# Performance work log

Measured on AMD Instinct MI355X. Metric: run time of the kernel, lower is better.

The kernel has to match this reference:

```python
import jax, jax.numpy as jnp
import numpy as np

P = 2048
D = 1024
H = 16
DH = D // H
HID = 32


def setup_inputs() -> dict:
    key = jax.random.key(0)
    ks = jax.random.split(key, 10)
    s = 0.02
    return {
        "x": jax.random.normal(ks[0], (P, D), jnp.float32),
        "rel": jax.random.normal(ks[1], (P, P, 2), jnp.float32),
        "w_qkv": jax.random.normal(ks[2], (D, 3 * D), jnp.float32) * s,
        "w_proj": jax.random.normal(ks[3], (D, D), jnp.float32) * s,
        "rpb_w1": jax.random.normal(ks[4], (2, HID), jnp.float32) * s,
        "rpb_b1": jnp.zeros((HID,), jnp.float32),
        "rpb_w2": jax.random.normal(ks[5], (HID, HID), jnp.float32) * s,
        "rpb_b2": jnp.zeros((HID,), jnp.float32),
        "rpb_w3": jax.random.normal(ks[6], (HID, 1), jnp.float32) * s,
        "rpb_b3": jnp.zeros((1,), jnp.float32),
    }


def reference(x, rel, w_qkv, w_proj, rpb_w1, rpb_b1, rpb_w2, rpb_b2, rpb_w3, rpb_b3):
    scale = 1.0 / np.sqrt(DH)
    qkv = x @ w_qkv                                   # [P, 3D]
    q, k, v = jnp.split(qkv, 3, axis=-1)
    # [P, D] -> [H, P, DH]
    q = q.reshape(P, H, DH).transpose(1, 0, 2)
    k = k.reshape(P, H, DH).transpose(1, 0, 2)
    v = v.reshape(P, H, DH).transpose(1, 0, 2)
    logits = jnp.einsum('hpd,hqd->hpq', q, k) * scale  # [H, P, P]
    # RelPosBias MLP: (dx,dy) -> scalar, applied over [P, P, 2]
    hcur = jax.nn.relu(rel @ rpb_w1 + rpb_b1)
    hcur = jax.nn.relu(hcur @ rpb_w2 + rpb_b2)
    bias = (hcur @ rpb_w3 + rpb_b3)[..., 0]            # [P, P]
    logits = logits + bias[None]
    attn = jax.nn.softmax(logits, axis=-1)
    out = jnp.einsum('hpq,hqd->hpd', attn, v)          # [H, P, DH]
    out = out.transpose(1, 0, 2).reshape(P, D)
    return out @ w_proj
```

## Files before the change

### kernel.cpp

```cpp
#include <hip/hip_runtime.h>
#include <hip/hip_bf16.h>
#include <type_traits>

typedef __attribute__((ext_vector_type(8))) short bf16x8;
typedef __attribute__((ext_vector_type(4))) float floatx4;
typedef __attribute__((ext_vector_type(2))) float float2v;

__device__ __forceinline__ float bf2f(unsigned short u) {
    union { unsigned int x; float f; } v; v.x = ((unsigned int)u) << 16; return v.f;
}
__device__ __forceinline__ unsigned short f2bf(float f) {
    union { float f; unsigned int u; } v; v.f = f;
    unsigned int x = v.u;
    unsigned int r = x + 0x7fffu + ((x >> 16) & 1u);
    return (unsigned short)(r >> 16);
}

typedef const __attribute__((address_space(1))) unsigned int u32_g;
typedef __attribute__((address_space(3))) unsigned int u32_l;
__device__ __forceinline__ void gld_lds16(const void* g, void* l) {
    __builtin_amdgcn_global_load_lds((u32_g*)g, (u32_l*)l, 16, 0, 0);
}

__device__ __forceinline__ void trans32(const float* __restrict__ in,
                                        unsigned short* __restrict__ out,
                                        int K, int N, int bx, int by,
                                        unsigned short (*T)[33]) {
    const int n0 = bx * 32, k0 = by * 32;
    const int r = threadIdx.x >> 3;
    const int c4 = (threadIdx.x & 7) * 4;
    float4 v = *reinterpret_cast<const float4*>(in + (size_t)(k0 + r) * N + n0 + c4);
    T[c4 + 0][r] = f2bf(v.x);
    T[c4 + 1][r] = f2bf(v.y);
    T[c4 + 2][r] = f2bf(v.z);
    T[c4 + 3][r] = f2bf(v.w);
    __syncthreads();
    ushort4 o = {T[r][c4], T[r][c4 + 1], T[r][c4 + 2], T[r][c4 + 3]};
    *reinterpret_cast<ushort4*>(out + (size_t)(n0 + r) * K + k0 + c4) = o;
}

__global__ __launch_bounds__(256) void prep(const float* __restrict__ x,
                                            unsigned short* __restrict__ xb,
                                            const float* __restrict__ wq,
                                            unsigned short* __restrict__ wqT,
                                            const float* __restrict__ wp,
                                            unsigned short* __restrict__ wpT) {
    __shared__ unsigned short T[32][33];
    const int b = blockIdx.x;
    if (b < 1024) {
        size_t i = ((size_t)b * 256 + threadIdx.x) * 8;
        float4 a = *reinterpret_cast<const float4*>(x + i);
        float4 c = *reinterpret_cast<const float4*>(x + i + 4);
        unsigned short t[8] = {f2bf(a.x), f2bf(a.y), f2bf(a.z), f2bf(a.w),
                               f2bf(c.x), f2bf(c.y), f2bf(c.z), f2bf(c.w)};
        *reinterpret_cast<uint4*>(xb + i) = *reinterpret_cast<const uint4*>(t);
    } else if (b < 4096) {
        int t = b - 1024;
        trans32(wq, wqT, 1024, 3072, t % 96, t / 96, T);
    } else {
        int t = b - 4096;
        trans32(wp, wpT, 1024, 1024, t % 32, t / 32, T);
    }
}

__global__ __launch_bounds__(256) void gemm128(const unsigned short* __restrict__ A,
                                               const unsigned short* __restrict__ Bt,
                                               unsigned short* __restrict__ C,
                                               int M, int N, int K) {
    __shared__ __align__(16) unsigned short As[128 * 32];
    __shared__ __align__(16) unsigned short Bs[128 * 32];

    const int tid = threadIdx.x;
    const int wave = tid >> 6;
    const int lane = tid & 63;
    const int m15 = lane & 15;
    const int quad = lane >> 4;
    const int wm = wave >> 1;
    const int wn = wave & 1;
    const int m0 = blockIdx.y * 128;
    const int n0 = blockIdx.x * 128;

    const int srow = lane >> 2;
    const int scol = (lane & 3) * 8;

    floatx4 acc[4][4];
#pragma unroll
    for (int mt = 0; mt < 4; mt++)
#pragma unroll
        for (int nt = 0; nt < 4; nt++) acc[mt][nt] = {0.f, 0.f, 0.f, 0.f};

    for (int k0 = 0; k0 < K; k0 += 32) {
#pragma unroll
        for (int i = 0; i < 2; i++) {
            int j = wave * 2 + i;
            gld_lds16(A + (size_t)(m0 + j * 16 + srow) * K + k0 + scol, &As[j * 16 * 32]);
            gld_lds16(Bt + (size_t)(n0 + j * 16 + srow) * K + k0 + scol, &Bs[j * 16 * 32]);
        }
        __syncthreads();

        bf16x8 a[4];
#pragma unroll
        for (int mt = 0; mt < 4; mt++)
            a[mt] = *reinterpret_cast<bf16x8*>(&As[(wm * 64 + mt * 16 + m15) * 32 + quad * 8]);
#pragma unroll
        for (int nt = 0; nt < 4; nt++) {
            bf16x8 b = *reinterpret_cast<bf16x8*>(&Bs[(wn * 64 + nt * 16 + m15) * 32 + quad * 8]);
#pragma unroll
            for (int mt = 0; mt < 4; mt++)
                acc[mt][nt] = __builtin_amdgcn_mfma_f32_16x16x32_bf16(a[mt], b, acc[mt][nt], 0, 0, 0);
        }
        __syncthreads();
    }

#pragma unroll
    for (int mt = 0; mt < 4; mt++)
#pragma unroll
        for (int nt = 0; nt < 4; nt++)
#pragma unroll
            for (int i = 0; i < 4; i++) {
                int row = m0 + wm * 64 + mt * 16 + quad * 4 + i;
                int col = n0 + wn * 64 + nt * 16 + m15;
                C[(size_t)row * N + col] = f2bf(acc[mt][nt][i]);
            }
}

template<int BN, typename TC>
__global__ __launch_bounds__(256) void gemm_abt(const unsigned short* __restrict__ A,
                                                const unsigned short* __restrict__ Bt,
                                                TC* __restrict__ C,
                                                int M, int N, int K) {
    constexpr int NT = BN / 32;
    __shared__ __align__(16) unsigned short As[64 * 32];
    __shared__ __align__(16) unsigned short Bs[BN * 32];

    const int tid = threadIdx.x;
    const int wave = tid >> 6;
    const int lane = tid & 63;
    const int m15 = lane & 15;
    const int quad = lane >> 4;
    const int wm = wave >> 1;
    const int wn = wave & 1;
    const int m0 = blockIdx.y * 64;
    const int n0 = blockIdx.x * BN;

    const int srow = lane >> 2;
    const int scol = (lane & 3) * 8;

    floatx4 acc[2][NT];
#pragma unroll
    for (int mt = 0; mt < 2; mt++)
#pragma unroll
        for (int nt = 0; nt < NT; nt++) acc[mt][nt] = {0.f, 0.f, 0.f, 0.f};

    for (int k0 = 0; k0 < K; k0 += 32) {
        gld_lds16(A + (size_t)(m0 + wave * 16 + srow) * K + k0 + scol, &As[wave * 16 * 32]);
#pragma unroll
        for (int i = 0; i < BN / 64; i++) {
            int j = wave * (BN / 64) + i;
            gld_lds16(Bt + (size_t)(n0 + j * 16 + srow) * K + k0 + scol, &Bs[j * 16 * 32]);
        }
        __syncthreads();

        bf16x8 a[2];
#pragma unroll
        for (int mt = 0; mt < 2; mt++)
            a[mt] = *reinterpret_cast<bf16x8*>(&As[(wm * 32 + mt * 16 + m15) * 32 + quad * 8]);
#pragma unroll
        for (int nt = 0; nt < NT; nt++) {
            bf16x8 b = *reinterpret_cast<bf16x8*>(&Bs[(wn * (BN / 2) + nt * 16 + m15) * 32 + quad * 8]);
#pragma unroll
            for (int mt = 0; mt < 2; mt++)
                acc[mt][nt] = __builtin_amdgcn_mfma_f32_16x16x32_bf16(a[mt], b, acc[mt][nt], 0, 0, 0);
        }
        __syncthreads();
    }

#pragma unroll
    for (int mt = 0; mt < 2; mt++)
#pragma unroll
        for (int nt = 0; nt < NT; nt++)
#pragma unroll
            for (int i = 0; i < 4; i++) {
                int row = m0 + wm * 32 + mt * 16 + quad * 4 + i;
                int col = n0 + wn * (BN / 2) + nt * 16 + m15;
                if constexpr (std::is_same<TC, float>::value)
                    C[(size_t)row * N + col] = acc[mt][nt][i];
                else
                    C[(size_t)row * N + col] = f2bf(acc[mt][nt][i]);
            }
}

__global__ __launch_bounds__(256) void rpb_mfma_kernel(const float* __restrict__ rel,
                                                       const float* __restrict__ w1,
                                                       const float* __restrict__ b1,
                                                       const float* __restrict__ w2,
                                                       const float* __restrict__ b2,
                                                       const float* __restrict__ w3,
                                                       const float* __restrict__ b3,
                                                       unsigned short* __restrict__ biasb) {
    const int tid = threadIdx.x;
    const int wave = tid >> 6;
    const int lane = tid & 63;
    const int m15 = lane & 15;
    const int quad = lane >> 4;

    bf16x8 af0, af1;
    {
        unsigned short t0[8], t1[8];
#pragma unroll
        for (int j = 0; j < 8; j++) {
            int k = quad * 8 + j;
            t0[j] = f2bf(w2[k * 32 + m15]);
            t1[j] = f2bf(w2[k * 32 + 16 + m15]);
        }
        af0 = *reinterpret_cast<bf16x8*>(t0);
        af1 = *reinterpret_cast<bf16x8*>(t1);
    }

    float2v w1a2[4], w1b2[4], b12[4];
#pragma unroll
    for (int p = 0; p < 4; p++) {
        int base = quad * 8 + 2 * p;
        w1a2[p] = {w1[base], w1[base + 1]};
        w1b2[p] = {w1[32 + base], w1[32 + base + 1]};
        b12[p]  = {b1[base], b1[base + 1]};
    }

    floatx4 b2r0, b2r1;
    float2v w3p00, w3p01, w3p10, w3p11;
    const float LOG2E = 1.44269504f;
    {
        float4 t0 = *reinterpret_cast<const float4*>(b2 + quad * 4);
        float4 t1 = *reinterpret_cast<const float4*>(b2 + 16 + quad * 4);
        b2r0 = {t0.x, t0.y, t0.z, t0.w};
        b2r1 = {t1.x, t1.y, t1.z, t1.w};
        float4 u0 = *reinterpret_cast<const float4*>(w3 + quad * 4);
        float4 u1 = *reinterpret_cast<const float4*>(w3 + 16 + quad * 4);
        w3p00 = {u0.x * LOG2E, u0.y * LOG2E};
        w3p01 = {u0.z * LOG2E, u0.w * LOG2E};
        w3p10 = {u1.x * LOG2E, u1.y * LOG2E};
        w3p11 = {u1.z * LOG2E, u1.w * LOG2E};
    }
    const float b3s = b3[0] * LOG2E;
    const float2v z2 = {0.f, 0.f};

    const int base = blockIdx.x * 1024 + wave * 64;

    for (int it = 0; it < 4; ++it) {
        const int pix0 = base + it * 256;
#pragma unroll
        for (int t = 0; t < 4; t++) {
            const int px = pix0 + t * 16;
            float2 dxy = *reinterpret_cast<const float2*>(rel + (size_t)(px + m15) * 2);
            float2v dx2 = {dxy.x, dxy.x}, dy2 = {dxy.y, dxy.y};

            unsigned int hp[4];
#pragma unroll
            for (int p = 0; p < 4; p++) {
                float2v h = __builtin_elementwise_fma(dx2, w1a2[p],
                             __builtin_elementwise_fma(dy2, w1b2[p], b12[p]));
                h = __builtin_elementwise_max(h, z2);
                hp[p] = __builtin_amdgcn_perm(__float_as_uint(h.y), __float_as_uint(h.x), 0x07060302u);
            }
            bf16x8 hb = *reinterpret_cast<bf16x8*>(hp);

            floatx4 d0 = __builtin_amdgcn_mfma_f32_16x16x32_bf16(af0, hb, b2r0, 0, 0, 0);
            floatx4 d1 = __builtin_amdgcn_mfma_f32_16x16x32_bf16(af1, hb, b2r1, 0, 0, 0);

            float2v m00 = __builtin_elementwise_max(__builtin_shufflevector(d0, d0, 0, 1), z2);
            float2v m01 = __builtin_elementwise_max(__builtin_shufflevector(d0, d0, 2, 3), z2);
            float2v m10 = __builtin_elementwise_max(__builtin_shufflevector(d1, d1, 0, 1), z2);
            float2v m11 = __builtin_elementwise_max(__builtin_shufflevector(d1, d1, 2, 3), z2);
            float2v acc2 = m00 * w3p00;
            acc2 = __builtin_elementwise_fma(m01, w3p01, acc2);
            acc2 = __builtin_elementwise_fma(m10, w3p10, acc2);
            acc2 = __builtin_elementwise_fma(m11, w3p11, acc2);
            float s = acc2.x + acc2.y;

            s += __shfl_xor(s, 16);
            s += __shfl_xor(s, 32);
            s += b3s;

            if (quad == t)
                biasb[(size_t)pix0 + m15 * 4 + t] = f2bf(s);
        }
    }
}

__global__ __launch_bounds__(512, 4) void attn_kernel(const unsigned short* __restrict__ qkv,
                                                      const unsigned short* __restrict__ biasb,
                                                      unsigned short* __restrict__ attn_out) {
    const int h = blockIdx.x;
    const int q0 = blockIdx.y * 64;
    __shared__ __align__(16) unsigned short Kst[2][64 * 72];
    __shared__ __align__(16) unsigned short Vst[2][64 * 72];
    __shared__ __align__(16) unsigned short Ps[8][16 * 72];

    const int tid = threadIdx.x;
    const int g = tid >> 8;
    const int w = (tid >> 6) & 3;
    const int lane = tid & 63;
    const int ltid = tid & 255;
    const int m15 = lane & 15;
    const int quad = lane >> 4;

    bf16x8 qf[2];
#pragma unroll
    for (int kh = 0; kh < 2; kh++)
        qf[kh] = *reinterpret_cast<const bf16x8*>(
            qkv + (size_t)(q0 + w * 16 + m15) * 3072 + h * 64 + kh * 32 + quad * 8);

    const int kr0 = ltid >> 3, kd0 = (ltid & 7) * 8;
    const int ka = (ltid & 31) * 2;
    const int vd0 = (ltid >> 5) * 8;

    unsigned short* Kc = Kst[g];
    unsigned short* Vc = Vst[g];
    const size_t kofs = (size_t)g * 1024;

    uint4 kreg0 = *reinterpret_cast<const uint4*>(qkv + (kofs + kr0) * 3072 + 1024 + h * 64 + kd0);
    uint4 kreg1 = *reinterpret_cast<const uint4*>(qkv + (kofs + kr0 + 32) * 3072 + 1024 + h * 64 + kd0);
    uint4 vrega = *reinterpret_cast<const uint4*>(qkv + (kofs + ka) * 3072 + 2048 + h * 64 + vd0);
    uint4 vregb = *reinterpret_cast<const uint4*>(qkv + (kofs + ka + 1) * 3072 + 2048 + h * 64 + vd0);

    unsigned short br[16];
#pragma unroll
    for (int i = 0; i < 4; i++) {
        ushort4 t = *reinterpret_cast<const ushort4*>(
            biasb + (size_t)(q0 + w * 16 + quad * 4 + i) * 2048 + kofs + m15 * 4);
        br[0 * 4 + i] = t.x; br[1 * 4 + i] = t.y; br[2 * 4 + i] = t.z; br[3 * 4 + i] = t.w;
    }

    float rs[4] = {0.f, 0.f, 0.f, 0.f};
    floatx4 acc[4];
#pragma unroll
    for (int i = 0; i < 4; i++) acc[i] = {0.f, 0.f, 0.f, 0.f};
    const float c1 = 0.125f * 1.44269504f;

    for (int kt = 0; kt < 16; ++kt) {
        __syncthreads();

        *reinterpret_cast<uint4*>(&Kc[kr0 * 72 + kd0]) = kreg0;
        *reinterpret_cast<uint4*>(&Kc[(kr0 + 32) * 72 + kd0]) = kreg1;
        {
            const unsigned int* aw = reinterpret_cast<const unsigned int*>(&vrega);
            const unsigned int* bw = reinterpret_cast<const unsigned int*>(&vregb);
#pragma unroll
            for (int wd = 0; wd < 4; wd++) {
                unsigned int lo = __builtin_amdgcn_perm(bw[wd], aw[wd], 0x05040100u);
                unsigned int hi = __builtin_amdgcn_perm(bw[wd], aw[wd], 0x07060302u);
                *reinterpret_cast<unsigned int*>(&Vc[(vd0 + 2 * wd) * 72 + ka]) = lo;
                *reinterpret_cast<unsigned int*>(&Vc[(vd0 + 2 * wd + 1) * 72 + ka]) = hi;
            }
        }
        __syncthreads();

        if (kt < 15) {
            const size_t kb = kofs + (size_t)(kt + 1) * 64;
            kreg0 = *reinterpret_cast<const uint4*>(qkv + (kb + kr0) * 3072 + 1024 + h * 64 + kd0);
            kreg1 = *reinterpret_cast<const uint4*>(qkv + (kb + kr0 + 32) * 3072 + 1024 + h * 64 + kd0);
            vrega = *reinterpret_cast<const uint4*>(qkv + (kb + ka) * 3072 + 2048 + h * 64 + vd0);
            vregb = *reinterpret_cast<const uint4*>(qkv + (kb + ka + 1) * 3072 + 2048 + h * 64 + vd0);
        }

        floatx4 s[4];
#pragma unroll
        for (int nt = 0; nt < 4; nt++) s[nt] = {0.f, 0.f, 0.f, 0.f};
#pragma unroll
        for (int kh = 0; kh < 2; kh++) {
#pragma unroll
            for (int nt = 0; nt < 4; nt++) {
                bf16x8 b = *reinterpret_cast<bf16x8*>(&Kc[(nt * 16 + m15) * 72 + kh * 32 + quad * 8]);
                s[nt] = __builtin_amdgcn_mfma_f32_16x16x32_bf16(qf[kh], b, s[nt], 0, 0, 0);
            }
        }

        float p[4][4];
#pragma unroll
        for (int nt = 0; nt < 4; nt++)
#pragma unroll
            for (int i = 0; i < 4; i++) {
                float lg = fmaf(s[nt][i], c1, bf2f(br[nt * 4 + i]));
                p[nt][i] = __builtin_amdgcn_exp2f(lg);
                rs[i] += p[nt][i];
            }

        if (kt < 15) {
            const size_t kb = kofs + (size_t)(kt + 1) * 64;
#pragma unroll
            for (int i = 0; i < 4; i++) {
                ushort4 t = *reinterpret_cast<const ushort4*>(
                    biasb + (size_t)(q0 + w * 16 + quad * 4 + i) * 2048 + kb + m15 * 4);
                br[0 * 4 + i] = t.x; br[1 * 4 + i] = t.y; br[2 * 4 + i] = t.z; br[3 * 4 + i] = t.w;
            }
        }

        unsigned short* Pw = Ps[tid >> 6];
#pragma unroll
        for (int nt = 0; nt < 4; nt++)
#pragma unroll
            for (int i = 0; i < 4; i++)
                Pw[(quad * 4 + i) * 72 + nt * 16 + m15] = f2bf(p[nt][i]);
        __asm__ volatile("s_waitcnt lgkmcnt(0)" ::: "memory");

#pragma unroll
        for (int kh = 0; kh < 2; kh++) {
            bf16x8 a = *reinterpret_cast<bf16x8*>(&Pw[m15 * 72 + kh * 32 + quad * 8]);
#pragma unroll
            for (int nt = 0; nt < 4; nt++) {
                bf16x8 b = *reinterpret_cast<bf16x8*>(&Vc[(nt * 16 + m15) * 72 + kh * 32 + quad * 8]);
                acc[nt] = __builtin_amdgcn_mfma_f32_16x16x32_bf16(a, b, acc[nt], 0, 0, 0);
            }
        }
    }

    float rsum[4];
#pragma unroll
    for (int i = 0; i < 4; i++) {
        float r = rs[i];
        r += __shfl_xor(r, 1);
        r += __shfl_xor(r, 2);
        r += __shfl_xor(r, 4);
        r += __shfl_xor(r, 8);
        rsum[i] = r;
    }

    float* accbuf = reinterpret_cast<float*>(&Kst[0][0]);
    float* lbuf = accbuf + 4096;

    __syncthreads();
    if (g == 1) {
#pragma unroll
        for (int nt = 0; nt < 4; nt++)
#pragma unroll
            for (int i = 0; i < 4; i++)
                accbuf[(w * 16 + quad * 4 + i) * 64 + nt * 16 + m15] = acc[nt][i];
        if (m15 == 0) {
#pragma unroll
            for (int i = 0; i < 4; i++) lbuf[w * 16 + quad * 4 + i] = rsum[i];
        }
    }
    __syncthreads();
    if (g == 0) {
        float linv[4];
#pragma unroll
        for (int i = 0; i < 4; i++)
            linv[i] = 1.f / (rsum[i] + lbuf[w * 16 + quad * 4 + i]);
#pragma unroll
        for (int nt = 0; nt < 4; nt++)
#pragma unroll
            for (int i = 0; i < 4; i++) {
                float o = (acc[nt][i] + accbuf[(w * 16 + quad * 4 + i) * 64 + nt * 16 + m15]) * linv[i];
                int row = q0 + w * 16 + quad * 4 + i;
                int col = h * 64 + nt * 16 + m15;
                attn_out[(size_t)row * 1024 + col] = f2bf(o);
            }
    }
}

extern "C" void kernel_launch(void* const* d_in, const int* in_sizes, int n_in,
                              void* d_out, int out_size, void* d_ws, size_t ws_size,
                              hipStream_t stream) {
    const float* x      = (const float*)d_in[0];
    const float* rel    = (const float*)d_in[1];
    const float* w_qkv  = (const float*)d_in[2];
    const float* w_proj = (const float*)d_in[3];
    const float* w1     = (const float*)d_in[4];
    const float* b1     = (const float*)d_in[5];
    const float* w2     = (const float*)d_in[6];
    const float* b2     = (const float*)d_in[7];
    const float* w3     = (const float*)d_in[8];
    const float* b3     = (const float*)d_in[9];

    char* ws = (char*)d_ws;
    unsigned short* qkv   = (unsigned short*)ws;
    unsigned short* biasb = (unsigned short*)(ws + 12582912);
    unsigned short* xb    = (unsigned short*)(ws + 20971520);
    unsigned short* attn  = xb;
    unsigned short* wqT   = (unsigned short*)(ws + 25165824);
    unsigned short* wpT   = (unsigned short*)(ws + 31457280);
    float* out = (float*)d_out;

    prep<<<5120, 256, 0, stream>>>(x, xb, w_qkv, wqT, w_proj, wpT);
    gemm128<<<dim3(24, 16), 256, 0, stream>>>(xb, wqT, qkv, 2048, 3072, 1024);
    rpb_mfma_kernel<<<4096, 256, 0, stream>>>(rel, w1, b1, w2, b2, w3, b3, biasb);
    attn_kernel<<<dim3(16, 32), 512, 0, stream>>>(qkv, biasb, attn);
    gemm_abt<64, float><<<dim3(16, 32), 256, 0, stream>>>(attn, wpT, out, 2048, 1024, 1024);
}
```

Before: 232.0 us.

## Merge QKV GEMM and RPB MLP into one launch; prefetch rel, MFMA reduction

Merges the QKV projection GEMM and the relative-position-bias MLP into a single kernel that picks its role by block index, so the 384 GEMM blocks and the 4096 bias blocks run concurrently and one launch is saved. Inside the bias path, the rel coordinates for the next iteration are prefetched into registers. The cross-quad shuffle reduction is replaced by an MFMA against a ones vector that also adds the final bias. The MFMA reduction rounds partial sums to bf16 before summing, which adds precision loss, and the GEMM shape is now hardcoded.

```diff
diff --git a/kernel.cpp b/kernel.cpp
--- a/kernel.cpp
+++ b/kernel.cpp
@@ -63,13 +63,11 @@
     }
 }
 
-__global__ __launch_bounds__(256) void gemm128(const unsigned short* __restrict__ A,
-                                               const unsigned short* __restrict__ Bt,
-                                               unsigned short* __restrict__ C,
-                                               int M, int N, int K) {
-    __shared__ __align__(16) unsigned short As[128 * 32];
-    __shared__ __align__(16) unsigned short Bs[128 * 32];
-
+__device__ __forceinline__ void gemm128_body(const unsigned short* __restrict__ A,
+                                             const unsigned short* __restrict__ Bt,
+                                             unsigned short* __restrict__ C,
+                                             int bx, int by,
+                                             unsigned short* As, unsigned short* Bs) {
     const int tid = threadIdx.x;
     const int wave = tid >> 6;
     const int lane = tid & 63;
@@ -77,9 +75,8 @@
     const int quad = lane >> 4;
     const int wm = wave >> 1;
     const int wn = wave & 1;
-    const int m0 = blockIdx.y * 128;
-    const int n0 = blockIdx.x * 128;
-
+    const int m0 = by * 128;
+    const int n0 = bx * 128;
     const int srow = lane >> 2;
     const int scol = (lane & 3) * 8;
 
@@ -89,12 +86,12 @@
 #pragma unroll
         for (int nt = 0; nt < 4; nt++) acc[mt][nt] = {0.f, 0.f, 0.f, 0.f};
 
-    for (int k0 = 0; k0 < K; k0 += 32) {
+    for (int k0 = 0; k0 < 1024; k0 += 32) {
 #pragma unroll
         for (int i = 0; i < 2; i++) {
             int j = wave * 2 + i;
-            gld_lds16(A + (size_t)(m0 + j * 16 + srow) * K + k0 + scol, &As[j * 16 * 32]);
-            gld_lds16(Bt + (size_t)(n0 + j * 16 + srow) * K + k0 + scol, &Bs[j * 16 * 32]);
+            gld_lds16(A + (size_t)(m0 + j * 16 + srow) * 1024 + k0 + scol, &As[j * 16 * 32]);
+            gld_lds16(Bt + (size_t)(n0 + j * 16 + srow) * 1024 + k0 + scol, &Bs[j * 16 * 32]);
         }
         __syncthreads();
 
@@ -120,84 +117,19 @@
             for (int i = 0; i < 4; i++) {
                 int row = m0 + wm * 64 + mt * 16 + quad * 4 + i;
                 int col = n0 + wn * 64 + nt * 16 + m15;
-                C[(size_t)row * N + col] = f2bf(acc[mt][nt][i]);
-            }
-}
-
-template<int BN, typename TC>
-__global__ __launch_bounds__(256) void gemm_abt(const unsigned short* __restrict__ A,
-                                                const unsigned short* __restrict__ Bt,
-                                                TC* __restrict__ C,
-                                                int M, int N, int K) {
-    constexpr int NT = BN / 32;
-    __shared__ __align__(16) unsigned short As[64 * 32];
-    __shared__ __align__(16) unsigned short Bs[BN * 32];
-
-    const int tid = threadIdx.x;
-    const int wave = tid >> 6;
-    const int lane = tid & 63;
-    const int m15 = lane & 15;
-    const int quad = lane >> 4;
-    const int wm = wave >> 1;
-    const int wn = wave & 1;
-    const int m0 = blockIdx.y * 64;
-    const int n0 = blockIdx.x * BN;
-
-    const int srow = lane >> 2;
-    const int scol = (lane & 3) * 8;
-
-    floatx4 acc[2][NT];
-#pragma unroll
-    for (int mt = 0; mt < 2; mt++)
-#pragma unroll
-        for (int nt = 0; nt < NT; nt++) acc[mt][nt] = {0.f, 0.f, 0.f, 0.f};
-
-    for (int k0 = 0; k0 < K; k0 += 32) {
-        gld_lds16(A + (size_t)(m0 + wave * 16 + srow) * K + k0 + scol, &As[wave * 16 * 32]);
-#pragma unroll
-        for (int i = 0; i < BN / 64; i++) {
-            int j = wave * (BN / 64) + i;
-            gld_lds16(Bt + (size_t)(n0 + j * 16 + srow) * K + k0 + scol, &Bs[j * 16 * 32]);
-        }
-        __syncthreads();
-
-        bf16x8 a[2];
-#pragma unroll
-        for (int mt = 0; mt < 2; mt++)
-            a[mt] = *reinterpret_cast<bf16x8*>(&As[(wm * 32 + mt * 16 + m15) * 32 + quad * 8]);
-#pragma unroll
-        for (int nt = 0; nt < NT; nt++) {
-            bf16x8 b = *reinterpret_cast<bf16x8*>(&Bs[(wn * (BN / 2) + nt * 16 + m15) * 32 + quad * 8]);
-#pragma unroll
-            for (int mt = 0; mt < 2; mt++)
-                acc[mt][nt] = __builtin_amdgcn_mfma_f32_16x16x32_bf16(a[mt], b, acc[mt][nt], 0, 0, 0);
-        }
-        __syncthreads();
-    }
-
-#pragma unroll
-    for (int mt = 0; mt < 2; mt++)
-#pragma unroll
-        for (int nt = 0; nt < NT; nt++)
-#pragma unroll
-            for (int i = 0; i < 4; i++) {
-                int row = m0 + wm * 32 + mt * 16 + quad * 4 + i;
-                int col = n0 + wn * (BN / 2) + nt * 16 + m15;
-                if constexpr (std::is_same<TC, float>::value)
-                    C[(size_t)row * N + col] = acc[mt][nt][i];
-                else
-                    C[(size_t)row * N + col] = f2bf(acc[mt][nt][i]);
-            }
-}
-
-__global__ __launch_bounds__(256) void rpb_mfma_kernel(const float* __restrict__ rel,
-                                                       const float* __restrict__ w1,
-                                                       const float* __restrict__ b1,
-                                                       const float* __restrict__ w2,
-                                                       const float* __restrict__ b2,
-                                                       const float* __restrict__ w3,
-                                                       const float* __restrict__ b3,
-                                                       unsigned short* __restrict__ biasb) {
+                C[(size_t)row * 3072 + col] = f2bf(acc[mt][nt][i]);
+            }
+}
+
+__device__ __forceinline__ void rpb_body(int bx,
+                                         const float* __restrict__ rel,
+                                         const float* __restrict__ w1,
+                                         const float* __restrict__ b1,
+                                         const float* __restrict__ w2,
+                                         const float* __restrict__ b2,
+                                         const float* __restrict__ w3,
+                                         const float* __restrict__ b3,
+                                         unsigned short* __restrict__ biasb) {
     const int tid = threadIdx.x;
     const int wave = tid >> 6;
     const int lane = tid & 63;
@@ -243,16 +175,33 @@
     }
     const float b3s = b3[0] * LOG2E;
     const float2v z2 = {0.f, 0.f};
-
-    const int base = blockIdx.x * 1024 + wave * 64;
+    const floatx4 b3r = {b3s, b3s, b3s, b3s};
+
+    bf16x8 ones;
+    {
+        unsigned int t[4] = {0x3f803f80u, 0x3f803f80u, 0x3f803f80u, 0x3f803f80u};
+        ones = *reinterpret_cast<bf16x8*>(t);
+    }
+
+    const int base = bx * 1024 + wave * 64;
+
+    float2 cur[4];
+#pragma unroll
+    for (int t = 0; t < 4; t++)
+        cur[t] = *reinterpret_cast<const float2*>(rel + (size_t)(base + t * 16 + m15) * 2);
 
     for (int it = 0; it < 4; ++it) {
         const int pix0 = base + it * 256;
+        float2 nxt[4];
+        if (it < 3) {
+#pragma unroll
+            for (int t = 0; t < 4; t++)
+                nxt[t] = *reinterpret_cast<const float2*>(rel + (size_t)(pix0 + 256 + t * 16 + m15) * 2);
+        }
+
 #pragma unroll
         for (int t = 0; t < 4; t++) {
-            const int px = pix0 + t * 16;
-            float2 dxy = *reinterpret_cast<const float2*>(rel + (size_t)(px + m15) * 2);
-            float2v dx2 = {dxy.x, dxy.x}, dy2 = {dxy.y, dxy.y};
+            float2v dx2 = {cur[t].x, cur[t].x}, dy2 = {cur[t].y, cur[t].y};
 
             unsigned int hp[4];
 #pragma unroll
@@ -277,14 +226,106 @@
             acc2 = __builtin_elementwise_fma(m11, w3p11, acc2);
             float s = acc2.x + acc2.y;
 
-            s += __shfl_xor(s, 16);
-            s += __shfl_xor(s, 32);
-            s += b3s;
+            unsigned int sb[4];
+            sb[0] = (unsigned int)f2bf(s);
+            sb[1] = 0; sb[2] = 0; sb[3] = 0;
+            bf16x8 sf = *reinterpret_cast<bf16x8*>(sb);
+            floatx4 dsum = __builtin_amdgcn_mfma_f32_16x16x32_bf16(ones, sf, b3r, 0, 0, 0);
 
             if (quad == t)
-                biasb[(size_t)pix0 + m15 * 4 + t] = f2bf(s);
-        }
-    }
+                biasb[(size_t)pix0 + m15 * 4 + t] = f2bf(dsum[0]);
+        }
+
+        if (it < 3) {
+#pragma unroll
+            for (int t = 0; t < 4; t++) cur[t] = nxt[t];
+        }
+    }
+}
+
+__global__ __launch_bounds__(256) void gemm_rpb(const unsigned short* __restrict__ xb,
+                                                const unsigned short* __restrict__ wqT,
+                                                unsigned short* __restrict__ qkv,
+                                                const float* __restrict__ rel,
+                                                const float* __restrict__ w1,
+                                                const float* __restrict__ b1,
+                                                const float* __restrict__ w2,
+                                                const float* __restrict__ b2,
+                                                const float* __restrict__ w3,
+                                                const float* __restrict__ b3,
+                                                unsigned short* __restrict__ biasb) {
+    __shared__ __align__(16) unsigned short S[2 * 128 * 32];
+    const int b = blockIdx.x;
+    if (b < 384)
+        gemm128_body(xb, wqT, qkv, b % 24, b / 24, S, S + 128 * 32);
+    else
+        rpb_body(b - 384, rel, w1, b1, w2, b2, w3, b3, biasb);
+}
+
+template<int BN, typename TC>
+__global__ __launch_bounds__(256) void gemm_abt(const unsigned short* __restrict__ A,
+                                                const unsigned short* __restrict__ Bt,
+                                                TC* __restrict__ C,
+                                                int M, int N, int K) {
+    constexpr int NT = BN / 32;
+    __shared__ __align__(16) unsigned short As[64 * 32];
+    __shared__ __align__(16) unsigned short Bs[BN * 32];
+
+    const int tid = threadIdx.x;
+    const int wave = tid >> 6;
+    const int lane = tid & 63;
+    const int m15 = lane & 15;
+    const int quad = lane >> 4;
+    const int wm = wave >> 1;
+    const int wn = wave & 1;
+    const int m0 = blockIdx.y * 64;
+    const int n0 = blockIdx.x * BN;
+
+    const int srow = lane >> 2;
+    const int scol = (lane & 3) * 8;
+
+    floatx4 acc[2][NT];
+#pragma unroll
+    for (int mt = 0; mt < 2; mt++)
+#pragma unroll
+        for (int nt = 0; nt < NT; nt++) acc[mt][nt] = {0.f, 0.f, 0.f, 0.f};
+
+    for (int k0 = 0; k0 < K; k0 += 32) {
+        gld_lds16(A + (size_t)(m0 + wave * 16 + srow) * K + k0 + scol, &As[wave * 16 * 32]);
+#pragma unroll
+        for (int i = 0; i < BN / 64; i++) {
+            int j = wave * (BN / 64) + i;
+            gld_lds16(Bt + (size_t)(n0 + j * 16 + srow) * K + k0 + scol, &Bs[j * 16 * 32]);
+        }
+        __syncthreads();
+
+        bf16x8 a[2];
+#pragma unroll
+        for (int mt = 0; mt < 2; mt++)
+            a[mt] = *reinterpret_cast<bf16x8*>(&As[(wm * 32 + mt * 16 + m15) * 32 + quad * 8]);
+#pragma unroll
+        for (int nt = 0; nt < NT; nt++) {
+            bf16x8 b = *reinterpret_cast<bf16x8*>(&Bs[(wn * (BN / 2) + nt * 16 + m15) * 32 + quad * 8]);
+#pragma unroll
+            for (int mt = 0; mt < 2; mt++)
+                acc[mt][nt] = __builtin_amdgcn_mfma_f32_16x16x32_bf16(a[mt], b, acc[mt][nt], 0, 0, 0);
+        }
+        __syncthreads();
+    }
+
+#pragma unroll
+    for (int mt = 0; mt < 2; mt++)
+#pragma unroll
+        for (int nt = 0; nt < NT; nt++)
+#pragma unroll
+            for (int i = 0; i < 4; i++) {
+                int row = m0 + wm * 32 + mt * 16 + quad * 4 + i;
+                int col = n0 + wn * (BN / 2) + nt * 16 + m15;
+                if constexpr (std::is_same<TC, float>::value)
+                    C[(size_t)row * N + col] = acc[mt][nt][i];
+                else
+                    C[(size_t)row * N + col] = f2bf(acc[mt][nt][i]);
+            }
 }
 
 __global__ __launch_bounds__(512, 4) void attn_kernel(const unsigned short* __restrict__ qkv,
@@ -482,8 +523,7 @@
     float* out = (float*)d_out;
 
     prep<<<5120, 256, 0, stream>>>(x, xb, w_qkv, wqT, w_proj, wpT);
-    gemm128<<<dim3(24, 16), 256, 0, stream>>>(xb, wqT, qkv, 2048, 3072, 1024);
-    rpb_mfma_kernel<<<4096, 256, 0, stream>>>(rel, w1, b1, w2, b2, w3, b3, biasb);
+    gemm_rpb<<<4480, 256, 0, stream>>>(xb, wqT, qkv, rel, w1, b1, w2, b2, w3, b3, biasb);
     attn_kernel<<<dim3(16, 32), 512, 0, stream>>>(qkv, biasb, attn);
     gemm_abt<64, float><<<dim3(16, 32), 256, 0, stream>>>(attn, wpT, out, 2048, 1024, 1024);
 }
```

Measured after the change: 213.0 us. 8.2% less time.
